# Optimization experiments

Hardware: AMD Instinct MI355X
Metric: run time of the kernel (lower is better)

The kernel has to match this reference:

```python
import jax, jax.numpy as jnp
import numpy as np

EMBED_DIM = 768
NUM_HEADS = 12
HEAD_DIM = EMBED_DIM // NUM_HEADS


def setup_inputs() -> dict:
    key = jax.random.key(0)
    k_x, k_wqkv, k_bqkv, k_wp, k_bp = jax.random.split(key, 5)
    B, N, C = 2, 2048, EMBED_DIM
    lim_qkv = 1.0 / np.sqrt(C)
    lim_p = 1.0 / np.sqrt(C)
    return {
        "x": jax.random.normal(k_x, (B, N, C), dtype=jnp.float32),
        # torch Linear weights: [out_features, in_features]
        "w_qkv": jax.random.uniform(k_wqkv, (3 * C, C), minval=-lim_qkv, maxval=lim_qkv, dtype=jnp.float32),
        "b_qkv": jax.random.uniform(k_bqkv, (3 * C,), minval=-lim_qkv, maxval=lim_qkv, dtype=jnp.float32),
        "w_proj": jax.random.uniform(k_wp, (C, C), minval=-lim_p, maxval=lim_p, dtype=jnp.float32),
        "b_proj": jax.random.uniform(k_bp, (C,), minval=-lim_p, maxval=lim_p, dtype=jnp.float32),
    }


def reference(x, w_qkv, b_qkv, w_proj, b_proj):
    b, n, c = x.shape
    h, d = NUM_HEADS, HEAD_DIM
    qkv = x @ w_qkv.T + b_qkv                      # [b, n, 3c]
    qkv = qkv.reshape(b, n, 3, h, d).transpose(2, 0, 3, 1, 4)  # [3, b, h, n, d]
    q, k, v = qkv[0], qkv[1], qkv[2]
    scale = d ** -0.5
    attn = jnp.einsum('bhnd,bhmd->bhnm', q, k) * scale  # [b, h, n, n]
    attn = jax.nn.softmax(attn, axis=-1)
    # dropout is identity at inference (eval mode)
    out = jnp.einsum('bhnm,bhmd->bhnd', attn, v)        # [b, h, n, d]
    out = out.transpose(0, 2, 1, 3).reshape(b, n, c)    # [b, n, c]
    return out @ w_proj.T + b_proj
```

## Files before the change

kernel.cpp:

```cpp
#include <hip/hip_runtime.h>
#include <cstdint>
#include <cstddef>

using u16    = uint16_t;
using u16x4  = __attribute__((ext_vector_type(4))) uint16_t;
using u16x8  = __attribute__((ext_vector_type(8))) uint16_t;
using bf16x2 = __attribute__((ext_vector_type(2))) __bf16;
using bf16x8 = __attribute__((ext_vector_type(8))) __bf16;
using f32x4  = __attribute__((ext_vector_type(4))) float;

__device__ __forceinline__ u16 f2b(float f) {
    union { float f; uint32_t u; } x; x.f = f;
    uint32_t r = x.u + 0x7FFFu + ((x.u >> 16) & 1u);
    return (u16)(r >> 16);
}
__device__ __forceinline__ uint32_t pk2(float a, float b) {
    bf16x2 t; t[0] = (__bf16)a; t[1] = (__bf16)b;
    return __builtin_bit_cast(uint32_t, t);
}
__device__ __forceinline__ bf16x8 ld8(const u16* p) {
    union { u16x8 v; u16x4 h[2]; } r;
    r.h[0] = *(const u16x4*)p;
    r.h[1] = *(const u16x4*)(p + 4);
    return __builtin_bit_cast(bf16x8, r.v);
}
__device__ __forceinline__ u16x8 ld8u(const u16* p) {
    union { u16x8 v; u16x4 h[2]; } r;
    r.h[0] = *(const u16x4*)p;
    r.h[1] = *(const u16x4*)(p + 4);
    return r.v;
}
__device__ __forceinline__ void st8(u16* p, u16x8 v) {
    union { u16x8 v; u16x4 h[2]; } r; r.v = v;
    *(u16x4*)p       = r.h[0];
    *(u16x4*)(p + 4) = r.h[1];
}

__device__ __forceinline__ void load16_async(const u16* g, u16* lds_base) {
    __builtin_amdgcn_global_load_lds(
        (const __attribute__((address_space(1))) u16*)g,
        (__attribute__((address_space(3))) u16*)(uint32_t)(uintptr_t)lds_base,
        16, 0, 0);
}

__global__ void conv_k(const float* __restrict__ x,  u16* __restrict__ xb,  int nx4,
                       const float* __restrict__ w1, u16* __restrict__ w1b, int n14,
                       const float* __restrict__ w2, u16* __restrict__ w2b, int n24)
{
    const int t   = blockIdx.x * blockDim.x + threadIdx.x;
    const int stp = gridDim.x * blockDim.x;
    for (int i = t; i < nx4; i += stp) {
        f32x4 v = ((const f32x4*)x)[i];
        u16x4 o;
        #pragma unroll
        for (int e = 0; e < 4; e++) o[e] = f2b(v[e]);
        ((u16x4*)xb)[i] = o;
    }
    for (int i = t; i < n14; i += stp) {
        f32x4 v = ((const f32x4*)w1)[i];
        u16x4 o;
        #pragma unroll
        for (int e = 0; e < 4; e++) o[e] = f2b(v[e]);
        ((u16x4*)w1b)[i] = o;
    }
    for (int i = t; i < n24; i += stp) {
        f32x4 v = ((const f32x4*)w2)[i];
        u16x4 o;
        #pragma unroll
        for (int e = 0; e < 4; e++) o[e] = f2b(v[e]);
        ((u16x4*)w2b)[i] = o;
    }
}

__global__ __launch_bounds__(256, 3) void gemm_qkv(
    const u16* __restrict__ A, const u16* __restrict__ W,
    const float* __restrict__ bias,
    u16* __restrict__ O0, u16* __restrict__ O1, u16* __restrict__ O2)
{
    __shared__ alignas(16) char smem[33792];
    u16* As = (u16*)smem;
    u16* Bs = (u16*)(smem + 8192);
    u16* T  = (u16*)smem;

    const int tid  = threadIdx.x;
    const int wid  = tid >> 6, lane = tid & 63;
    const int quad = lane >> 4, lc = lane & 15;
    const int row0 = blockIdx.x * 128, col0 = blockIdx.y * 128;
    const int wm   = (wid >> 1) * 64, wn = (wid & 1) * 64;

    const int srA = wid * 32 + (lane >> 2);
    const int scA = (lane & 3) * 8;

    f32x4 acc[4][4] = {};

    for (int k0 = 0; k0 < 768; k0 += 32) {
        __syncthreads();
        #pragma unroll
        for (int t = 0; t < 2; t++) {
            load16_async(&A[(row0 + srA + t*16) * 768 + k0 + scA], &As[wid*1024 + t*512]);
            load16_async(&W[(col0 + srA + t*16) * 768 + k0 + scA], &Bs[wid*1024 + t*512]);
        }
        __syncthreads();

        bf16x8 a[4], b[4];
        #pragma unroll
        for (int i = 0; i < 4; i++)
            a[i] = __builtin_bit_cast(bf16x8, *(const u16x8*)&As[(wm + i*16 + lc)*32 + quad*8]);
        #pragma unroll
        for (int j = 0; j < 4; j++)
            b[j] = __builtin_bit_cast(bf16x8, *(const u16x8*)&Bs[(wn + j*16 + lc)*32 + quad*8]);
        #pragma unroll
        for (int i = 0; i < 4; i++)
            #pragma unroll
            for (int j = 0; j < 4; j++)
                acc[i][j] = __builtin_amdgcn_mfma_f32_16x16x32_bf16(a[i], b[j], acc[i][j], 0, 0, 0);
    }

    if (col0 < 1536) {
        #pragma unroll
        for (int i = 0; i < 4; i++) {
            #pragma unroll
            for (int j = 0; j < 4; j++) {
                const int gc = col0 + wn + j*16 + lc;
                const float bv = bias[gc];
                #pragma unroll
                for (int r = 0; r < 4; r++) {
                    const int gr = row0 + wm + i*16 + quad*4 + r;
                    const u16 ob = f2b(acc[i][j][r] + bv);
                    if (gc < 768) O0[gr * 768 + gc] = ob;
                    else          O1[gr * 768 + (gc - 768)] = ob;
                }
            }
        }
    } else {
        __syncthreads();
        #pragma unroll
        for (int j = 0; j < 4; j++) {
            const int cl = wn + j*16 + lc;
            const float bv = bias[col0 + cl];
            #pragma unroll
            for (int i = 0; i < 4; i++) {
                uint2 w;
                w.x = pk2(acc[i][j][0] + bv, acc[i][j][1] + bv);
                w.y = pk2(acc[i][j][2] + bv, acc[i][j][3] + bv);
                *(uint2*)&T[cl*132 + wm + i*16 + quad*4] = w;
            }
        }
        __syncthreads();

        const int cl = tid >> 1;
        const int sg = (tid & 1) * 64;
        const int c2 = (col0 - 1536) + cl;
        const int hh = c2 >> 6, dd = c2 & 63;
        const int bb = row0 >> 11, nn0 = row0 & 2047;
        u16* dst = &O2[((size_t)((bb*12 + hh)*64 + dd))*2048 + nn0 + sg];
        #pragma unroll
        for (int k = 0; k < 8; k++)
            *(u16x8*)&dst[k*8] = ld8u(&T[cl*132 + sg + k*8]);
    }
}

__global__ __launch_bounds__(256, 4) void gemm_proj(
    const u16* __restrict__ A, const u16* __restrict__ W,
    const float* __restrict__ bias, float* __restrict__ F0)
{
    __shared__ alignas(16) u16 As[64 * 32];
    __shared__ alignas(16) u16 Bs[64 * 32];
    const int tid  = threadIdx.x;
    const int wid  = tid >> 6, lane = tid & 63;
    const int quad = lane >> 4, lc = lane & 15;
    const int row0 = blockIdx.x * 64, col0 = blockIdx.y * 64;
    const int wm   = (wid >> 1) * 32, wn = (wid & 1) * 32;

    const int srA = wid * 16 + (lane >> 2);
    const int scA = (lane & 3) * 8;

    f32x4 acc[2][2] = {};

    for (int k0 = 0; k0 < 768; k0 += 32) {
        __syncthreads();
        load16_async(&A[(row0 + srA) * 768 + k0 + scA], &As[wid*512]);
        load16_async(&W[(col0 + srA) * 768 + k0 + scA], &Bs[wid*512]);
        __syncthreads();

        bf16x8 a[2], b[2];
        #pragma unroll
        for (int i = 0; i < 2; i++)
            a[i] = __builtin_bit_cast(bf16x8, *(const u16x8*)&As[(wm + i*16 + lc)*32 + quad*8]);
        #pragma unroll
        for (int j = 0; j < 2; j++)
            b[j] = __builtin_bit_cast(bf16x8, *(const u16x8*)&Bs[(wn + j*16 + lc)*32 + quad*8]);
        #pragma unroll
        for (int i = 0; i < 2; i++)
            #pragma unroll
            for (int j = 0; j < 2; j++)
                acc[i][j] = __builtin_amdgcn_mfma_f32_16x16x32_bf16(a[i], b[j], acc[i][j], 0, 0, 0);
    }

    #pragma unroll
    for (int i = 0; i < 2; i++)
        #pragma unroll
        for (int j = 0; j < 2; j++) {
            const int gc = col0 + wn + j*16 + lc;
            const float bv = bias[gc];
            #pragma unroll
            for (int r = 0; r < 4; r++) {
                const int gr = row0 + wm + i*16 + quad*4 + r;
                F0[gr * 768 + gc] = acc[i][j][r] + bv;
            }
        }
}

__global__ __launch_bounds__(256, 3) void attn_k(
    const u16* __restrict__ Q, const u16* __restrict__ K,
    const u16* __restrict__ V, u16* __restrict__ O)
{
    __shared__ alignas(16) char lds[53760];
    u16* Ks = (u16*)(lds);
    u16* Vs = (u16*)(lds + 17408);
    u16* Ps = (u16*)(lds + 35328);
    float* Obuf = (float*)(lds);
    float* Lbuf = (float*)(lds + 35328);

    const int tid  = threadIdx.x;
    const int wid  = tid >> 6, lane = tid & 63;
    const int quad = lane >> 4, lc = lane & 15;
    const int li = blockIdx.x;
    const int bh = li >> 5, qt = li & 31;
    const int b = bh / 12, h = bh - b * 12;
    const int q0 = qt * 64;

    const u16* Qp = Q + ((size_t)b * 2048) * 768 + h * 64;
    const u16* Kp = K + ((size_t)b * 2048) * 768 + h * 64;
    const u16* Vp = V + (size_t)bh * 64 * 2048;
    u16*       Op = O + ((size_t)b * 2048) * 768 + h * 64;

    bf16x8 qf[4][2];
    #pragma unroll
    for (int qg = 0; qg < 4; qg++)
        #pragma unroll
        for (int kb = 0; kb < 2; kb++) {
            u16x8 t = *(const u16x8*)&Qp[(q0 + qg*16 + lc) * 768 + kb*32 + quad*8];
            bf16x8 sc;
            #pragma unroll
            for (int e = 0; e < 8; e++) {
                union { uint32_t u; float f; } z; z.u = ((uint32_t)t[e]) << 16;
                sc[e] = (__bf16)(z.f * 0.125f);
            }
            qf[qg][kb] = sc;
        }

    float l_[4] = {};
    f32x4 o_[2][4] = {};

    const int kr = tid >> 3, kseg = (tid & 7) * 8;
    const int vr = tid >> 4, vseg = (tid & 15) * 8;
    const int kb0   = wid * 32;
    const int kh    = wid >> 1;
    const int dbase = (wid & 1) * 32;

    u16x8 kpre[4], vpre[4];
    #pragma unroll
    for (int p = 0; p < 4; p++)
        kpre[p] = *(const u16x8*)&Kp[(kr + p*32)*768 + kseg];
    #pragma unroll
    for (int p = 0; p < 4; p++)
        vpre[p] = *(const u16x8*)&Vp[(vr + p*16)*2048 + vseg];

    for (int kt = 0; kt < 16; kt++) {
        __syncthreads();
        #pragma unroll
        for (int p = 0; p < 4; p++)
            st8(&Ks[(kr + p*32)*68 + kseg], kpre[p]);
        #pragma unroll
        for (int p = 0; p < 4; p++)
            st8(&Vs[(vr + p*16)*140 + vseg], vpre[p]);
        __syncthreads();

        if (kt < 15) {
            #pragma unroll
            for (int p = 0; p < 4; p++)
                kpre[p] = *(const u16x8*)&Kp[((kt+1)*128 + kr + p*32)*768 + kseg];
            #pragma unroll
            for (int p = 0; p < 4; p++)
                vpre[p] = *(const u16x8*)&Vp[(vr + p*16)*2048 + (kt+1)*128 + vseg];
        }

        f32x4 s[2][4] = {};
        __builtin_amdgcn_s_setprio(1);
        #pragma unroll
        for (int g = 0; g < 2; g++) {
            bf16x8 k0f = ld8(&Ks[(kb0 + g*16 + lc)*68 + quad*8]);
            bf16x8 k1f = ld8(&Ks[(kb0 + g*16 + lc)*68 + 32 + quad*8]);
            #pragma unroll
            for (int qg = 0; qg < 4; qg++) {
                s[g][qg] = __builtin_amdgcn_mfma_f32_16x16x32_bf16(k0f, qf[qg][0], s[g][qg], 0, 0, 0);
                s[g][qg] = __builtin_amdgcn_mfma_f32_16x16x32_bf16(k1f, qf[qg][1], s[g][qg], 0, 0, 0);
            }
        }
        __builtin_amdgcn_s_setprio(0);

        #pragma unroll
        for (int g = 0; g < 2; g++)
            #pragma unroll
            for (int qg = 0; qg < 4; qg++)
                #pragma unroll
                for (int r = 0; r < 4; r++) {
                    float p = __expf(s[g][qg][r]);
                    s[g][qg][r] = p;
                    l_[qg] += p;
                }

        #pragma unroll
        for (int g = 0; g < 2; g++)
            #pragma unroll
            for (int qg = 0; qg < 4; qg++) {
                uint2 w;
                w.x = pk2(s[g][qg][0], s[g][qg][1]);
                w.y = pk2(s[g][qg][2], s[g][qg][3]);
                *(uint2*)&Ps[(wid*64 + qg*16 + lc)*36 + g*16 + quad*4] = w;
            }

        __syncthreads();

        #pragma unroll
        for (int kb = 0; kb < 2; kb++) {
            const int pw = kh*2 + kb;
            bf16x8 pf[4], vf[2];
            #pragma unroll
            for (int qg = 0; qg < 4; qg++)
                pf[qg] = ld8(&Ps[(pw*64 + qg*16 + lc)*36 + quad*8]);
            #pragma unroll
            for (int dg = 0; dg < 2; dg++)
                vf[dg] = ld8(&Vs[(dbase + dg*16 + lc)*140 + kh*64 + kb*32 + quad*8]);
            __builtin_amdgcn_s_setprio(1);
            #pragma unroll
            for (int dg = 0; dg < 2; dg++)
                #pragma unroll
                for (int qg = 0; qg < 4; qg++)
                    o_[dg][qg] = __builtin_amdgcn_mfma_f32_16x16x32_bf16(vf[dg], pf[qg], o_[dg][qg], 0, 0, 0);
            __builtin_amdgcn_s_setprio(0);
        }
    }

    #pragma unroll
    for (int qg = 0; qg < 4; qg++) {
        l_[qg] += __shfl_xor(l_[qg], 16);
        l_[qg] += __shfl_xor(l_[qg], 32);
    }
    __syncthreads();
    if (quad == 0)
        #pragma unroll
        for (int qg = 0; qg < 4; qg++)
            Lbuf[wid*64 + qg*16 + lc] = l_[qg];

    #pragma unroll
    for (int dg = 0; dg < 2; dg++)
        #pragma unroll
        for (int qg = 0; qg < 4; qg++)
            #pragma unroll
            for (int r = 0; r < 4; r++)
                Obuf[(wid*32 + dg*16 + quad*4 + r)*65 + qg*16 + lc] = o_[dg][qg][r];
    __syncthreads();

    const int eq = tid & 63;
    const int es = tid >> 6;
    const float linv = 1.0f / (Lbuf[0*64 + eq] + Lbuf[1*64 + eq] +
                               Lbuf[2*64 + eq] + Lbuf[3*64 + eq]);
    const int dh = es >> 1;
    const int dl = (es & 1) * 16;
    const int r0 = dh * 32 * 65, r1 = (dh + 2) * 32 * 65;

    u16x8 ov0, ov1;
    #pragma unroll
    for (int j = 0; j < 8; j++) {
        const float sum = Obuf[r0 + (dl + j)*65 + eq] + Obuf[r1 + (dl + j)*65 + eq];
        ov0[j] = f2b(sum * linv);
    }
    #pragma unroll
    for (int j = 0; j < 8; j++) {
        const float sum = Obuf[r0 + (dl + 8 + j)*65 + eq] + Obuf[r1 + (dl + 8 + j)*65 + eq];
        ov1[j] = f2b(sum * linv);
    }
    *(u16x8*)&Op[(size_t)(q0 + eq) * 768 + es*16]     = ov0;
    *(u16x8*)&Op[(size_t)(q0 + eq) * 768 + es*16 + 8] = ov1;
}

extern "C" void kernel_launch(void* const* d_in, const int* in_sizes, int n_in,
                              void* d_out, int out_size, void* d_ws, size_t ws_size,
                              hipStream_t stream)
{
    const float* x    = (const float*)d_in[0];
    const float* wqkv = (const float*)d_in[1];
    const float* bqkv = (const float*)d_in[2];
    const float* wp   = (const float*)d_in[3];
    const float* bp   = (const float*)d_in[4];
    float* out = (float*)d_out;
    char* ws = (char*)d_ws;

    u16* Qw    = (u16*)(ws);
    u16* Vt    = (u16*)(ws + 6291456);
    u16* wqkvb = (u16*)(ws + 12582912);
    u16* wpb   = (u16*)(ws + 16121856);
    u16* Kw    = (u16*)d_out;
    u16* xb    = (u16*)((char*)d_out + 6291456);

    conv_k<<<512, 256, 0, stream>>>(x, xb, 3145728/4, wqkv, wqkvb, 1769472/4, wp, wpb, 589824/4);
    gemm_qkv<<<dim3(32, 18), 256, 0, stream>>>(xb, wqkvb, bqkv, Qw, Kw, Vt);
    attn_k<<<768, 256, 0, stream>>>(Qw, Kw, Vt, Qw);
    gemm_proj<<<dim3(64, 12), 256, 0, stream>>>(Qw, wpb, bp, out);
}
```

Measured before the change: 156.4 us.

## Widen GEMM K-tile to 64 with XOR-swizzled LDS and use exp2 softmax

Both the QKV and projection GEMMs now stage a 64-wide K slice per iteration instead of 32. Global-to-LDS loads use an XOR swizzle on the 16-byte chunk column so the strided fragment reads avoid LDS bank conflicts. This halves the number of barrier pairs per GEMM. In attention, the log2(e) factor is folded into the Q scale and the exponential becomes a native exp2, removing a multiply per score. It also adds bf16 rounding of Q with a different scale, which slightly changes numerics.

```diff
diff --git a/kernel.cpp b/kernel.cpp
--- a/kernel.cpp
+++ b/kernel.cpp
@@ -34,6 +34,13 @@
     union { u16x8 v; u16x4 h[2]; } r; r.v = v;
     *(u16x4*)p       = r.h[0];
     *(u16x4*)(p + 4) = r.h[1];
+}
+__device__ __forceinline__ float ex2(float x) {
+#if __has_builtin(__builtin_amdgcn_exp2f)
+    return __builtin_amdgcn_exp2f(x);
+#else
+    return __expf(x * 0.6931471805599453f);
+#endif
 }
 
 __device__ __forceinline__ void load16_async(const u16* g, u16* lds_base) {
@@ -79,7 +86,7 @@
 {
     __shared__ alignas(16) char smem[33792];
     u16* As = (u16*)smem;
-    u16* Bs = (u16*)(smem + 8192);
+    u16* Bs = (u16*)(smem + 16384);
     u16* T  = (u16*)smem;
 
     const int tid  = threadIdx.x;
@@ -88,32 +95,39 @@
     const int row0 = blockIdx.x * 128, col0 = blockIdx.y * 128;
     const int wm   = (wid >> 1) * 64, wn = (wid & 1) * 64;
 
-    const int srA = wid * 32 + (lane >> 2);
-    const int scA = (lane & 3) * 8;
+    const int srA = wid * 8 + (lane >> 3);
+    const int scA = ((lane & 7) ^ ((lane >> 3) & 7)) * 8;
+
+    const int rc0 = ((0*4 + quad) ^ (lc & 7)) * 8;
+    const int rc1 = ((1*4 + quad) ^ (lc & 7)) * 8;
 
     f32x4 acc[4][4] = {};
 
-    for (int k0 = 0; k0 < 768; k0 += 32) {
-        __syncthreads();
-        #pragma unroll
-        for (int t = 0; t < 2; t++) {
-            load16_async(&A[(row0 + srA + t*16) * 768 + k0 + scA], &As[wid*1024 + t*512]);
-            load16_async(&W[(col0 + srA + t*16) * 768 + k0 + scA], &Bs[wid*1024 + t*512]);
-        }
-        __syncthreads();
-
-        bf16x8 a[4], b[4];
-        #pragma unroll
-        for (int i = 0; i < 4; i++)
-            a[i] = __builtin_bit_cast(bf16x8, *(const u16x8*)&As[(wm + i*16 + lc)*32 + quad*8]);
-        #pragma unroll
-        for (int j = 0; j < 4; j++)
-            b[j] = __builtin_bit_cast(bf16x8, *(const u16x8*)&Bs[(wn + j*16 + lc)*32 + quad*8]);
-        #pragma unroll
-        for (int i = 0; i < 4; i++)
+    for (int k0 = 0; k0 < 768; k0 += 64) {
+        __syncthreads();
+        #pragma unroll
+        for (int c = 0; c < 4; c++) {
+            load16_async(&A[(row0 + c*32 + srA) * 768 + k0 + scA], &As[(c*32 + wid*8) * 64]);
+            load16_async(&W[(col0 + c*32 + srA) * 768 + k0 + scA], &Bs[(c*32 + wid*8) * 64]);
+        }
+        __syncthreads();
+
+        #pragma unroll
+        for (int s = 0; s < 2; s++) {
+            const int rc = s ? rc1 : rc0;
+            bf16x8 a[4], b[4];
+            #pragma unroll
+            for (int i = 0; i < 4; i++)
+                a[i] = __builtin_bit_cast(bf16x8, *(const u16x8*)&As[(wm + i*16 + lc)*64 + rc]);
             #pragma unroll
             for (int j = 0; j < 4; j++)
-                acc[i][j] = __builtin_amdgcn_mfma_f32_16x16x32_bf16(a[i], b[j], acc[i][j], 0, 0, 0);
+                b[j] = __builtin_bit_cast(bf16x8, *(const u16x8*)&Bs[(wn + j*16 + lc)*64 + rc]);
+            #pragma unroll
+            for (int i = 0; i < 4; i++)
+                #pragma unroll
+                for (int j = 0; j < 4; j++)
+                    acc[i][j] = __builtin_amdgcn_mfma_f32_16x16x32_bf16(a[i], b[j], acc[i][j], 0, 0, 0);
+        }
     }
 
     if (col0 < 1536) {
@@ -164,37 +178,46 @@
     const u16* __restrict__ A, const u16* __restrict__ W,
     const float* __restrict__ bias, float* __restrict__ F0)
 {
-    __shared__ alignas(16) u16 As[64 * 32];
-    __shared__ alignas(16) u16 Bs[64 * 32];
+    __shared__ alignas(16) u16 As[64 * 64];
+    __shared__ alignas(16) u16 Bs[64 * 64];
     const int tid  = threadIdx.x;
     const int wid  = tid >> 6, lane = tid & 63;
     const int quad = lane >> 4, lc = lane & 15;
     const int row0 = blockIdx.x * 64, col0 = blockIdx.y * 64;
     const int wm   = (wid >> 1) * 32, wn = (wid & 1) * 32;
 
-    const int srA = wid * 16 + (lane >> 2);
-    const int scA = (lane & 3) * 8;
+    const int srA = wid * 8 + (lane >> 3);
+    const int scA = ((lane & 7) ^ ((lane >> 3) & 7)) * 8;
+    const int rc0 = ((0*4 + quad) ^ (lc & 7)) * 8;
+    const int rc1 = ((1*4 + quad) ^ (lc & 7)) * 8;
 
     f32x4 acc[2][2] = {};
 
-    for (int k0 = 0; k0 < 768; k0 += 32) {
-        __syncthreads();
-        load16_async(&A[(row0 + srA) * 768 + k0 + scA], &As[wid*512]);
-        load16_async(&W[(col0 + srA) * 768 + k0 + scA], &Bs[wid*512]);
-        __syncthreads();
-
-        bf16x8 a[2], b[2];
-        #pragma unroll
-        for (int i = 0; i < 2; i++)
-            a[i] = __builtin_bit_cast(bf16x8, *(const u16x8*)&As[(wm + i*16 + lc)*32 + quad*8]);
-        #pragma unroll
-        for (int j = 0; j < 2; j++)
-            b[j] = __builtin_bit_cast(bf16x8, *(const u16x8*)&Bs[(wn + j*16 + lc)*32 + quad*8]);
-        #pragma unroll
-        for (int i = 0; i < 2; i++)
+    for (int k0 = 0; k0 < 768; k0 += 64) {
+        __syncthreads();
+        #pragma unroll
+        for (int c = 0; c < 2; c++) {
+            load16_async(&A[(row0 + c*32 + srA) * 768 + k0 + scA], &As[(c*32 + wid*8) * 64]);
+            load16_async(&W[(col0 + c*32 + srA) * 768 + k0 + scA], &Bs[(c*32 + wid*8) * 64]);
+        }
+        __syncthreads();
+
+        #pragma unroll
+        for (int s = 0; s < 2; s++) {
+            const int rc = s ? rc1 : rc0;
+            bf16x8 a[2], b[2];
+            #pragma unroll
+            for (int i = 0; i < 2; i++)
+                a[i] = __builtin_bit_cast(bf16x8, *(const u16x8*)&As[(wm + i*16 + lc)*64 + rc]);
             #pragma unroll
             for (int j = 0; j < 2; j++)
-                acc[i][j] = __builtin_amdgcn_mfma_f32_16x16x32_bf16(a[i], b[j], acc[i][j], 0, 0, 0);
+                b[j] = __builtin_bit_cast(bf16x8, *(const u16x8*)&Bs[(wn + j*16 + lc)*64 + rc]);
+            #pragma unroll
+            for (int i = 0; i < 2; i++)
+                #pragma unroll
+                for (int j = 0; j < 2; j++)
+                    acc[i][j] = __builtin_amdgcn_mfma_f32_16x16x32_bf16(a[i], b[j], acc[i][j], 0, 0, 0);
+        }
     }
 
     #pragma unroll
@@ -235,6 +258,7 @@
     const u16* Vp = V + (size_t)bh * 64 * 2048;
     u16*       Op = O + ((size_t)b * 2048) * 768 + h * 64;
 
+    const float qs = 0.125f * 1.4426950408889634f;
     bf16x8 qf[4][2];
     #pragma unroll
     for (int qg = 0; qg < 4; qg++)
@@ -245,7 +269,7 @@
             #pragma unroll
             for (int e = 0; e < 8; e++) {
                 union { uint32_t u; float f; } z; z.u = ((uint32_t)t[e]) << 16;
-                sc[e] = (__bf16)(z.f * 0.125f);
+                sc[e] = (__bf16)(z.f * qs);
             }
             qf[qg][kb] = sc;
         }
@@ -306,7 +330,7 @@
             for (int qg = 0; qg < 4; qg++)
                 #pragma unroll
                 for (int r = 0; r < 4; r++) {
-                    float p = __expf(s[g][qg][r]);
+                    float p = ex2(s[g][qg][r]);
                     s[g][qg][r] = p;
                     l_[qg] += p;
                 }
```

Result: faster. 151.2 us (-3.3%).
